# Kernel optimization log

Measured on AMD Instinct MI355X. Metric: run time of the kernel, lower is better.

## Reference

```python
import jax, jax.numpy as jnp
import numpy as np

N_NODES = 100000
DIM = 128
N_EDGES = 1600000
BN_EPS = 1e-5


def setup_inputs() -> dict:
    key = jax.random.key(0)
    ks = jax.random.split(key, 8)
    x = jax.random.normal(ks[0], (N_NODES, DIM), dtype=jnp.float32)
    ei = jax.random.randint(ks[1], (2, N_EDGES), 0, N_NODES, dtype=jnp.int32)
    # GINConv train_eps scalar
    eps = jnp.zeros((), dtype=jnp.float32)
    # MLP: Linear(dim, 2*dim) -> BN(2*dim) -> ReLU -> Dropout -> Linear(2*dim, dim) -> BN(dim) -> ReLU
    s1 = 1.0 / np.sqrt(DIM)
    s2 = 1.0 / np.sqrt(2 * DIM)
    W1 = jax.random.uniform(ks[2], (DIM, 2 * DIM), jnp.float32, -s1, s1)
    b1 = jax.random.uniform(ks[3], (2 * DIM,), jnp.float32, -s1, s1)
    W2 = jax.random.uniform(ks[4], (2 * DIM, DIM), jnp.float32, -s2, s2)
    b2 = jax.random.uniform(ks[5], (DIM,), jnp.float32, -s2, s2)
    g1 = jnp.ones((2 * DIM,), jnp.float32)
    be1 = jnp.zeros((2 * DIM,), jnp.float32)
    m1 = jax.random.normal(ks[6], (2 * DIM,), jnp.float32) * 0.1
    v1 = jnp.ones((2 * DIM,), jnp.float32)
    g2 = jnp.ones((DIM,), jnp.float32)
    be2 = jnp.zeros((DIM,), jnp.float32)
    m2 = jax.random.normal(ks[7], (DIM,), jnp.float32) * 0.1
    v2 = jnp.ones((DIM,), jnp.float32)
    return {"x": x, "eps": eps, "W1": W1, "b1": b1, "g1": g1, "be1": be1,
            "m1": m1, "v1": v1, "W2": W2, "b2": b2, "g2": g2, "be2": be2,
            "m2": m2, "v2": v2, "ei": ei}


def _bn(h, gamma, beta, mean, var):
    # BatchNorm1d in eval mode (running stats)
    return gamma * (h - mean) * jax.lax.rsqrt(var + BN_EPS) + beta


def reference(x, eps, W1, b1, g1, be1, m1, v1, W2, b2, g2, be2, m2, v2, ei):
    src, dst = ei[0], ei[1]
    # GIN aggregation: sum of neighbor (source) features scattered to destination
    agg = jax.ops.segment_sum(x[src], dst, num_segments=N_NODES)  # [N, dim]
    h = (1.0 + eps) * x + agg
    h = jax.nn.relu(_bn(h @ W1 + b1, g1, be1, m1, v1))  # [N, 2*dim]
    # Dropout is identity in eval mode
    h = jax.nn.relu(_bn(h @ W2 + b2, g2, be2, m2, v2))  # [N, dim]
    return h
```

## Files before the change

### kernel.cpp

```cpp
#include <hip/hip_runtime.h>

#define N_NODES 100000
#define DIM     128
#define HID     256
#define BN_EPS  1e-5f
#define TILES   3125
#define GEMM_GRID 256
#define BK_BITS 9
#define NBK     196
#define BKCAP   12288
#define EPB     4096

typedef _Float16     half4  __attribute__((ext_vector_type(4)));
typedef _Float16     half8  __attribute__((ext_vector_type(8)));
typedef float        f32x4  __attribute__((ext_vector_type(4)));

static __device__ __forceinline__ f32x4 mfma16h(half8 a, half8 b, f32x4 c) {
    return __builtin_amdgcn_mfma_f32_16x16x32_f16(a, b, c, 0, 0, 0);
}

__global__ __launch_bounds__(256) void cvt_kernel(const float* __restrict__ x,
                                                  _Float16* __restrict__ x16) {
    int i = blockIdx.x * 256 + threadIdx.x;
    float4 v = ((const float4*)x)[i];
    half4 o;
    o[0] = (_Float16)v.x; o[1] = (_Float16)v.y;
    o[2] = (_Float16)v.z; o[3] = (_Float16)v.w;
    ((half4*)x16)[i] = o;
}

__global__ __launch_bounds__(256) void binscatter_kernel(
    const int* __restrict__ src, const int* __restrict__ dst,
    int* __restrict__ cursor, unsigned int* __restrict__ pairs, int nE) {
    __shared__ int cnt[NBK];
    __shared__ int gbase[NBK];
    int t = threadIdx.x;
    for (int i = t; i < NBK; i += 256) cnt[i] = 0;
    __syncthreads();
    int e0 = blockIdx.x * EPB;
    int n = min(EPB, nE - e0);
    int d[16];
#pragma unroll
    for (int k = 0; k < 16; ++k) {
        int idx = t + k * 256;
        if (idx < n) {
            d[k] = dst[e0 + idx];
            atomicAdd(&cnt[d[k] >> BK_BITS], 1);
        }
    }
    __syncthreads();
    for (int i = t; i < NBK; i += 256) {
        int c = cnt[i];
        gbase[i] = c ? atomicAdd(&cursor[i], c) : 0;
    }
    __syncthreads();
    for (int i = t; i < NBK; i += 256) cnt[i] = 0;
    __syncthreads();
#pragma unroll
    for (int k = 0; k < 16; ++k) {
        int idx = t + k * 256;
        if (idx < n) {
            int b = d[k] >> BK_BITS;
            int r = atomicAdd(&cnt[b], 1);
            pairs[(long long)b * BKCAP + gbase[b] + r] =
                ((unsigned)src[e0 + idx] << BK_BITS) | ((unsigned)d[k] & 511u);
        }
    }
}

__global__ __launch_bounds__(256) void bscan_kernel(const int* __restrict__ cursor,
                                                    int* __restrict__ bbase) {
    __shared__ int tmp[256];
    int t = threadIdx.x;
    int v = (t < NBK) ? cursor[t] : 0;
    tmp[t] = v;
    __syncthreads();
    for (int s = 1; s < 256; s <<= 1) {
        int a = (t >= s) ? tmp[t - s] : 0;
        __syncthreads();
        tmp[t] += a;
        __syncthreads();
    }
    if (t < NBK) bbase[t] = tmp[t] - v;
}

__global__ __launch_bounds__(512) void bucket_fill_kernel(
    const unsigned int* __restrict__ pairs, const int* __restrict__ cursor,
    const int* __restrict__ bbase, int* __restrict__ rowptr, int* __restrict__ csr_src) {
    __shared__ int cnt[512];
    __shared__ int off[512];
    int b = blockIdx.x;
    int t = threadIdx.x;
    int nd0 = b << BK_BITS;
    int nn = min(512, N_NODES - nd0);
    int m = cursor[b];
    int base = bbase[b];
    const unsigned int* bp = pairs + (long long)b * BKCAP;
    cnt[t] = 0;
    __syncthreads();
    for (int e = t; e < m; e += 512)
        atomicAdd(&cnt[bp[e] & 511u], 1);
    __syncthreads();
    int v = cnt[t];
    off[t] = v;
    __syncthreads();
    for (int s = 1; s < 512; s <<= 1) {
        int a = (t >= s) ? off[t - s] : 0;
        __syncthreads();
        off[t] += a;
        __syncthreads();
    }
    int excl = off[t] - v;
    __syncthreads();
    off[t] = excl;
    if (t < nn) rowptr[nd0 + t] = base + excl;
    if (b == NBK - 1 && t == 0) rowptr[N_NODES] = base + m;
    cnt[t] = 0;
    __syncthreads();
    for (int e = t; e < m; e += 512) {
        unsigned int p = bp[e];
        int li = p & 511u;
        int r = atomicAdd(&cnt[li], 1);
        csr_src[base + off[li] + r] = (int)(p >> BK_BITS);
    }
}

__global__ __launch_bounds__(256) void gather_pack_kernel(
    const float* __restrict__ x, const _Float16* __restrict__ x16,
    const float* __restrict__ epsp, const int* __restrict__ rowptr,
    const int* __restrict__ csr_src, _Float16* __restrict__ h16) {
    int node = blockIdx.x * 8 + (threadIdx.x >> 5);
    int lane = threadIdx.x & 31;
    const half4* xp = (const half4*)x16;
    int beg = rowptr[node], end = rowptr[node + 1];
    float4 a0 = {0.f,0.f,0.f,0.f}, a1 = {0.f,0.f,0.f,0.f};
    float4 a2 = {0.f,0.f,0.f,0.f}, a3 = {0.f,0.f,0.f,0.f};
#define ACC4(A, V) { A.x += (float)V[0]; A.y += (float)V[1]; A.z += (float)V[2]; A.w += (float)V[3]; }
    int j = beg;
    for (; j + 4 <= end; j += 4) {
        int s0 = csr_src[j], s1 = csr_src[j+1], s2 = csr_src[j+2], s3 = csr_src[j+3];
        half4 v0 = xp[s0 * 32 + lane];
        half4 v1 = xp[s1 * 32 + lane];
        half4 v2 = xp[s2 * 32 + lane];
        half4 v3 = xp[s3 * 32 + lane];
        ACC4(a0, v0); ACC4(a1, v1); ACC4(a2, v2); ACC4(a3, v3);
    }
    for (; j < end; ++j) {
        int s = csr_src[j];
        half4 v = xp[s * 32 + lane];
        ACC4(a0, v);
    }
#undef ACC4
    float sc = 1.f + epsp[0];
    float4 xv = ((const float4*)x)[node * 32 + lane];
    half4 o;
    o[0] = (_Float16)fmaf(sc, xv.x, a0.x + a1.x + a2.x + a3.x);
    o[1] = (_Float16)fmaf(sc, xv.y, a0.y + a1.y + a2.y + a3.y);
    o[2] = (_Float16)fmaf(sc, xv.z, a0.z + a1.z + a2.z + a3.z);
    o[3] = (_Float16)fmaf(sc, xv.w, a0.w + a1.w + a2.w + a3.w);
    ((half4*)h16)[node * 32 + lane] = o;
}

__global__ __launch_bounds__(512, 2) void gemm1_kernel(
    const _Float16* __restrict__ h16, const float* __restrict__ W1,
    const float* __restrict__ b1, const float* __restrict__ g1,
    const float* __restrict__ be1, const float* __restrict__ m1,
    const float* __restrict__ v1, _Float16* __restrict__ h1p) {
    int t = threadIdx.x;
    int w = t >> 6, l = t & 63;
    int l15 = l & 15, q = l >> 4;
    int cg = w & 3, mg = w >> 2;

    half8 B1h[4][4], B1l[4][4];
    float s1v[4], sh1v[4];
#pragma unroll
    for (int nt = 0; nt < 4; ++nt) {
        int col = 64 * cg + 16 * nt + l15;
#pragma unroll
        for (int ks = 0; ks < 4; ++ks) {
            half8 bh, bl;
#pragma unroll
            for (int i = 0; i < 8; ++i) {
                float wv = W1[(32 * ks + 8 * q + i) * HID + col];
                _Float16 hh = (_Float16)wv;
                bh[i] = hh;
                bl[i] = (_Float16)(wv - (float)hh);
            }
            B1h[nt][ks] = bh; B1l[nt][ks] = bl;
        }
        float sc = g1[col] * rsqrtf(v1[col] + BN_EPS);
        s1v[nt] = sc;
        sh1v[nt] = (b1[col] - m1[col]) * sc + be1[col];
    }

    for (int tile = blockIdx.x; tile < TILES; tile += GEMM_GRID) {
        int row0 = tile * 32;
        int row = row0 + 16 * mg + l15;
        const _Float16* arow = h16 + (long long)row * DIM;
        half8 A[4];
#pragma unroll
        for (int ks = 0; ks < 4; ++ks) A[ks] = *(const half8*)(arow + 32 * ks + 8 * q);
        f32x4 acc[4];
#pragma unroll
        for (int nt = 0; nt < 4; ++nt) acc[nt] = (f32x4)(0.f);
#pragma unroll
        for (int nt = 0; nt < 4; ++nt)
#pragma unroll
            for (int ks = 0; ks < 4; ++ks) {
                acc[nt] = mfma16h(A[ks], B1h[nt][ks], acc[nt]);
                acc[nt] = mfma16h(A[ks], B1l[nt][ks], acc[nt]);
            }
#pragma unroll
        for (int nt = 0; nt < 4; ++nt) {
            int col = 64 * cg + 16 * nt + l15;
#pragma unroll
            for (int reg = 0; reg < 4; ++reg) {
                int orow = row0 + 16 * mg + 4 * q + reg;
                float vv = fmaxf(0.f, fmaf(acc[nt][reg], s1v[nt], sh1v[nt]));
                h1p[(long long)orow * HID + col] = (_Float16)vv;
            }
        }
    }
}

__global__ __launch_bounds__(512, 2) void gemm2_kernel(
    const _Float16* __restrict__ h1p, const float* __restrict__ W2,
    const float* __restrict__ b2, const float* __restrict__ g2,
    const float* __restrict__ be2, const float* __restrict__ m2,
    const float* __restrict__ v2, float* __restrict__ out) {
    int t = threadIdx.x;
    int w = t >> 6, l = t & 63;
    int l15 = l & 15, q = l >> 4;
    int cg = w & 3, mg = w >> 2;

    half8 B2h[2][8], B2l[2][8];
    float s2v[2], sh2v[2];
#pragma unroll
    for (int nt = 0; nt < 2; ++nt) {
        int col = 32 * cg + 16 * nt + l15;
#pragma unroll
        for (int ks = 0; ks < 8; ++ks) {
            half8 bh, bl;
#pragma unroll
            for (int i = 0; i < 8; ++i) {
                float wv = W2[(32 * ks + 8 * q + i) * DIM + col];
                _Float16 hh = (_Float16)wv;
                bh[i] = hh;
                bl[i] = (_Float16)(wv - (float)hh);
            }
            B2h[nt][ks] = bh; B2l[nt][ks] = bl;
        }
        float sc = g2[col] * rsqrtf(v2[col] + BN_EPS);
        s2v[nt] = sc;
        sh2v[nt] = (b2[col] - m2[col]) * sc + be2[col];
    }

    for (int tile = blockIdx.x; tile < TILES; tile += GEMM_GRID) {
        int row0 = tile * 32;
        int row = row0 + 16 * mg + l15;
        const _Float16* arow = h1p + (long long)row * HID;
        half8 A2[8];
#pragma unroll
        for (int ks = 0; ks < 8; ++ks) A2[ks] = *(const half8*)(arow + 32 * ks + 8 * q);
        f32x4 acc[2];
        acc[0] = (f32x4)(0.f); acc[1] = (f32x4)(0.f);
#pragma unroll
        for (int nt = 0; nt < 2; ++nt)
#pragma unroll
            for (int ks = 0; ks < 8; ++ks) {
                acc[nt] = mfma16h(A2[ks], B2h[nt][ks], acc[nt]);
                acc[nt] = mfma16h(A2[ks], B2l[nt][ks], acc[nt]);
            }
#pragma unroll
        for (int nt = 0; nt < 2; ++nt) {
            int col = 32 * cg + 16 * nt + l15;
#pragma unroll
            for (int reg = 0; reg < 4; ++reg) {
                int orow = row0 + 16 * mg + 4 * q + reg;
                out[(long long)orow * DIM + col] = fmaxf(0.f, fmaf(acc[nt][reg], s2v[nt], sh2v[nt]));
            }
        }
    }
}

extern "C" void kernel_launch(void* const* d_in, const int* in_sizes, int n_in,
                              void* d_out, int out_size, void* d_ws, size_t ws_size,
                              hipStream_t stream) {
    const float* x   = (const float*)d_in[0];
    const float* eps = (const float*)d_in[1];
    const float* W1  = (const float*)d_in[2];
    const float* b1  = (const float*)d_in[3];
    const float* g1  = (const float*)d_in[4];
    const float* be1 = (const float*)d_in[5];
    const float* m1  = (const float*)d_in[6];
    const float* v1  = (const float*)d_in[7];
    const float* W2  = (const float*)d_in[8];
    const float* b2  = (const float*)d_in[9];
    const float* g2  = (const float*)d_in[10];
    const float* be2 = (const float*)d_in[11];
    const float* m2  = (const float*)d_in[12];
    const float* v2  = (const float*)d_in[13];
    const int*   ei  = (const int*)d_in[14];
    int nE = in_sizes[14] / 2;
    const int* src = ei;
    const int* dst = ei + nE;

    char* ws = (char*)d_ws;
    int*          cursor  = (int*)(ws + 0);
    int*          bbase   = (int*)(ws + 1024);
    int*          rowptr  = (int*)(ws + 4096);
    int*          csr_src = (int*)(ws + 405504);
    unsigned int* pairs   = (unsigned int*)(ws + 6806528);
    _Float16*     x16     = (_Float16*)(ws + 16441344);
    _Float16*     h1p     = (_Float16*)ws;

    _Float16* h16 = (_Float16*)d_out;

    cvt_kernel<<<N_NODES * DIM / 4 / 256, 256, 0, stream>>>(x, x16);

    hipMemsetAsync(cursor, 0, NBK * sizeof(int), stream);
    binscatter_kernel<<<(nE + EPB - 1) / EPB, 256, 0, stream>>>(src, dst, cursor, pairs, nE);
    bscan_kernel<<<1, 256, 0, stream>>>(cursor, bbase);
    bucket_fill_kernel<<<NBK, 512, 0, stream>>>(pairs, cursor, bbase, rowptr, csr_src);

    gather_pack_kernel<<<N_NODES / 8, 256, 0, stream>>>(x, x16, eps, rowptr, csr_src, h16);

    gemm1_kernel<<<GEMM_GRID, 512, 0, stream>>>(h16, W1, b1, g1, be1, m1, v1, h1p);

    gemm2_kernel<<<GEMM_GRID, 512, 0, stream>>>(h1p, W2, b2, g2, be2, m2, v2, (float*)d_out);
}
```

Measured before the change: 179.1 us.

## Fuse MLP GEMMs via LDS, merge cvt into binning, drop split-fp16 weights

Both GEMMs now run in one kernel, with the hidden activation tile staged in swizzled shared memory instead of written to and reread from global memory. The fp32 to fp16 conversion runs as extra blocks of the binning kernel. The bucket-offset scan moves into bucket_fill, removing a launch. The gather uses 16 lanes with half8 loads per node. The hi/lo split-weight MFMA pair is dropped for a single fp16 weight, which halves MFMA work but lowers weight precision and may affect accuracy.

```diff
diff --git a/kernel.cpp b/kernel.cpp
--- a/kernel.cpp
+++ b/kernel.cpp
@@ -10,8 +10,9 @@
 #define NBK     196
 #define BKCAP   12288
 #define EPB     4096
-
-typedef _Float16     half4  __attribute__((ext_vector_type(4)));
+#define BIN_BLOCKS 391
+#define CVT_BLOCKS 3125
+
 typedef _Float16     half8  __attribute__((ext_vector_type(8)));
 typedef float        f32x4  __attribute__((ext_vector_type(4)));
 
@@ -19,22 +20,32 @@
     return __builtin_amdgcn_mfma_f32_16x16x32_f16(a, b, c, 0, 0, 0);
 }
 
-__global__ __launch_bounds__(256) void cvt_kernel(const float* __restrict__ x,
-                                                  _Float16* __restrict__ x16) {
-    int i = blockIdx.x * 256 + threadIdx.x;
-    float4 v = ((const float4*)x)[i];
-    half4 o;
-    o[0] = (_Float16)v.x; o[1] = (_Float16)v.y;
-    o[2] = (_Float16)v.z; o[3] = (_Float16)v.w;
-    ((half4*)x16)[i] = o;
-}
-
-__global__ __launch_bounds__(256) void binscatter_kernel(
+__global__ __launch_bounds__(256) void bin_cvt_kernel(
     const int* __restrict__ src, const int* __restrict__ dst,
-    int* __restrict__ cursor, unsigned int* __restrict__ pairs, int nE) {
+    int* __restrict__ cursor, unsigned int* __restrict__ pairs, int nE,
+    const float* __restrict__ x, _Float16* __restrict__ x16) {
+    int t = threadIdx.x;
+    if (blockIdx.x >= BIN_BLOCKS) {
+        int bc = blockIdx.x - BIN_BLOCKS;
+#pragma unroll
+        for (int k = 0; k < 4; ++k) {
+            int i = bc * 1024 + k * 256 + t;
+            float4 v = ((const float4*)x)[i];
+            half8 o8;
+            _Float16 h0 = (_Float16)v.x, h1 = (_Float16)v.y,
+                     h2 = (_Float16)v.z, h3 = (_Float16)v.w;
+            unsigned long long pk =
+                (unsigned long long)__builtin_bit_cast(unsigned short, h0)
+              | ((unsigned long long)__builtin_bit_cast(unsigned short, h1) << 16)
+              | ((unsigned long long)__builtin_bit_cast(unsigned short, h2) << 32)
+              | ((unsigned long long)__builtin_bit_cast(unsigned short, h3) << 48);
+            ((unsigned long long*)x16)[i] = pk;
+            (void)o8;
+        }
+        return;
+    }
     __shared__ int cnt[NBK];
     __shared__ int gbase[NBK];
-    int t = threadIdx.x;
     for (int i = t; i < NBK; i += 256) cnt[i] = 0;
     __syncthreads();
     int e0 = blockIdx.x * EPB;
@@ -68,33 +79,29 @@
     }
 }
 
-__global__ __launch_bounds__(256) void bscan_kernel(const int* __restrict__ cursor,
-                                                    int* __restrict__ bbase) {
-    __shared__ int tmp[256];
-    int t = threadIdx.x;
-    int v = (t < NBK) ? cursor[t] : 0;
-    tmp[t] = v;
-    __syncthreads();
-    for (int s = 1; s < 256; s <<= 1) {
-        int a = (t >= s) ? tmp[t - s] : 0;
-        __syncthreads();
-        tmp[t] += a;
-        __syncthreads();
-    }
-    if (t < NBK) bbase[t] = tmp[t] - v;
-}
-
 __global__ __launch_bounds__(512) void bucket_fill_kernel(
     const unsigned int* __restrict__ pairs, const int* __restrict__ cursor,
-    const int* __restrict__ bbase, int* __restrict__ rowptr, int* __restrict__ csr_src) {
+    int* __restrict__ rowptr, int* __restrict__ csr_src) {
     __shared__ int cnt[512];
     __shared__ int off[512];
+    __shared__ int stmp[256];
+    __shared__ int s_base;
     int b = blockIdx.x;
     int t = threadIdx.x;
+    if (t < 256) stmp[t] = (t < NBK) ? cursor[t] : 0;
+    __syncthreads();
+    for (int s = 1; s < 256; s <<= 1) {
+        int a = (t >= s && t < 256) ? stmp[t - s] : 0;
+        __syncthreads();
+        if (t < 256) stmp[t] += a;
+        __syncthreads();
+    }
+    if (t == 0) s_base = stmp[b] - cursor[b];
+    __syncthreads();
+    int base = s_base;
+    int m = cursor[b];
     int nd0 = b << BK_BITS;
     int nn = min(512, N_NODES - nd0);
-    int m = cursor[b];
-    int base = bbase[b];
     const unsigned int* bp = pairs + (long long)b * BKCAP;
     cnt[t] = 0;
     __syncthreads();
@@ -125,130 +132,92 @@
     }
 }
 
-__global__ __launch_bounds__(256) void gather_pack_kernel(
+__global__ __launch_bounds__(256) void gather_kernel(
     const float* __restrict__ x, const _Float16* __restrict__ x16,
     const float* __restrict__ epsp, const int* __restrict__ rowptr,
     const int* __restrict__ csr_src, _Float16* __restrict__ h16) {
-    int node = blockIdx.x * 8 + (threadIdx.x >> 5);
-    int lane = threadIdx.x & 31;
-    const half4* xp = (const half4*)x16;
+    int node = blockIdx.x * 16 + (threadIdx.x >> 4);
+    int lane = threadIdx.x & 15;
+    const half8* xp = (const half8*)x16;
     int beg = rowptr[node], end = rowptr[node + 1];
-    float4 a0 = {0.f,0.f,0.f,0.f}, a1 = {0.f,0.f,0.f,0.f};
-    float4 a2 = {0.f,0.f,0.f,0.f}, a3 = {0.f,0.f,0.f,0.f};
-#define ACC4(A, V) { A.x += (float)V[0]; A.y += (float)V[1]; A.z += (float)V[2]; A.w += (float)V[3]; }
+    float s0[8] = {0,0,0,0,0,0,0,0}, s1[8] = {0,0,0,0,0,0,0,0};
     int j = beg;
     for (; j + 4 <= end; j += 4) {
-        int s0 = csr_src[j], s1 = csr_src[j+1], s2 = csr_src[j+2], s3 = csr_src[j+3];
-        half4 v0 = xp[s0 * 32 + lane];
-        half4 v1 = xp[s1 * 32 + lane];
-        half4 v2 = xp[s2 * 32 + lane];
-        half4 v3 = xp[s3 * 32 + lane];
-        ACC4(a0, v0); ACC4(a1, v1); ACC4(a2, v2); ACC4(a3, v3);
+        int n0 = csr_src[j], n1 = csr_src[j+1], n2 = csr_src[j+2], n3 = csr_src[j+3];
+        half8 v0 = xp[n0 * 16 + lane];
+        half8 v1 = xp[n1 * 16 + lane];
+        half8 v2 = xp[n2 * 16 + lane];
+        half8 v3 = xp[n3 * 16 + lane];
+#pragma unroll
+        for (int i = 0; i < 8; ++i) {
+            s0[i] += (float)v0[i]; s1[i] += (float)v1[i];
+            s0[i] += (float)v2[i]; s1[i] += (float)v3[i];
+        }
     }
     for (; j < end; ++j) {
-        int s = csr_src[j];
-        half4 v = xp[s * 32 + lane];
-        ACC4(a0, v);
-    }
-#undef ACC4
+        half8 v = xp[csr_src[j] * 16 + lane];
+#pragma unroll
+        for (int i = 0; i < 8; ++i) s0[i] += (float)v[i];
+    }
     float sc = 1.f + epsp[0];
-    float4 xv = ((const float4*)x)[node * 32 + lane];
-    half4 o;
-    o[0] = (_Float16)fmaf(sc, xv.x, a0.x + a1.x + a2.x + a3.x);
-    o[1] = (_Float16)fmaf(sc, xv.y, a0.y + a1.y + a2.y + a3.y);
-    o[2] = (_Float16)fmaf(sc, xv.z, a0.z + a1.z + a2.z + a3.z);
-    o[3] = (_Float16)fmaf(sc, xv.w, a0.w + a1.w + a2.w + a3.w);
-    ((half4*)h16)[node * 32 + lane] = o;
-}
-
-__global__ __launch_bounds__(512, 2) void gemm1_kernel(
-    const _Float16* __restrict__ h16, const float* __restrict__ W1,
-    const float* __restrict__ b1, const float* __restrict__ g1,
-    const float* __restrict__ be1, const float* __restrict__ m1,
-    const float* __restrict__ v1, _Float16* __restrict__ h1p) {
+    float4 xa = ((const float4*)x)[node * 32 + lane * 2];
+    float4 xb = ((const float4*)x)[node * 32 + lane * 2 + 1];
+    half8 o;
+    o[0] = (_Float16)fmaf(sc, xa.x, s0[0] + s1[0]);
+    o[1] = (_Float16)fmaf(sc, xa.y, s0[1] + s1[1]);
+    o[2] = (_Float16)fmaf(sc, xa.z, s0[2] + s1[2]);
+    o[3] = (_Float16)fmaf(sc, xa.w, s0[3] + s1[3]);
+    o[4] = (_Float16)fmaf(sc, xb.x, s0[4] + s1[4]);
+    o[5] = (_Float16)fmaf(sc, xb.y, s0[5] + s1[5]);
+    o[6] = (_Float16)fmaf(sc, xb.z, s0[6] + s1[6]);
+    o[7] = (_Float16)fmaf(sc, xb.w, s0[7] + s1[7]);
+    ((half8*)h16)[node * 16 + lane] = o;
+}
+
+__global__ __launch_bounds__(512, 2) void mlp_fused_kernel(
+    const _Float16* __restrict__ h16,
+    const float* __restrict__ W1, const float* __restrict__ b1,
+    const float* __restrict__ g1, const float* __restrict__ be1,
+    const float* __restrict__ m1, const float* __restrict__ v1,
+    const float* __restrict__ W2, const float* __restrict__ b2,
+    const float* __restrict__ g2, const float* __restrict__ be2,
+    const float* __restrict__ m2, const float* __restrict__ v2,
+    float* __restrict__ out) {
+    __shared__ _Float16 sh1[32 * HID];
     int t = threadIdx.x;
     int w = t >> 6, l = t & 63;
     int l15 = l & 15, q = l >> 4;
     int cg = w & 3, mg = w >> 2;
 
-    half8 B1h[4][4], B1l[4][4];
+    half8 B1[4][4];
     float s1v[4], sh1v[4];
 #pragma unroll
     for (int nt = 0; nt < 4; ++nt) {
         int col = 64 * cg + 16 * nt + l15;
 #pragma unroll
         for (int ks = 0; ks < 4; ++ks) {
-            half8 bh, bl;
-#pragma unroll
-            for (int i = 0; i < 8; ++i) {
-                float wv = W1[(32 * ks + 8 * q + i) * HID + col];
-                _Float16 hh = (_Float16)wv;
-                bh[i] = hh;
-                bl[i] = (_Float16)(wv - (float)hh);
-            }
-            B1h[nt][ks] = bh; B1l[nt][ks] = bl;
+            half8 bh;
+#pragma unroll
+            for (int i = 0; i < 8; ++i)
+                bh[i] = (_Float16)W1[(32 * ks + 8 * q + i) * HID + col];
+            B1[nt][ks] = bh;
         }
         float sc = g1[col] * rsqrtf(v1[col] + BN_EPS);
         s1v[nt] = sc;
         sh1v[nt] = (b1[col] - m1[col]) * sc + be1[col];
     }
-
-    for (int tile = blockIdx.x; tile < TILES; tile += GEMM_GRID) {
-        int row0 = tile * 32;
-        int row = row0 + 16 * mg + l15;
-        const _Float16* arow = h16 + (long long)row * DIM;
-        half8 A[4];
-#pragma unroll
-        for (int ks = 0; ks < 4; ++ks) A[ks] = *(const half8*)(arow + 32 * ks + 8 * q);
-        f32x4 acc[4];
-#pragma unroll
-        for (int nt = 0; nt < 4; ++nt) acc[nt] = (f32x4)(0.f);
-#pragma unroll
-        for (int nt = 0; nt < 4; ++nt)
-#pragma unroll
-            for (int ks = 0; ks < 4; ++ks) {
-                acc[nt] = mfma16h(A[ks], B1h[nt][ks], acc[nt]);
-                acc[nt] = mfma16h(A[ks], B1l[nt][ks], acc[nt]);
-            }
-#pragma unroll
-        for (int nt = 0; nt < 4; ++nt) {
-            int col = 64 * cg + 16 * nt + l15;
-#pragma unroll
-            for (int reg = 0; reg < 4; ++reg) {
-                int orow = row0 + 16 * mg + 4 * q + reg;
-                float vv = fmaxf(0.f, fmaf(acc[nt][reg], s1v[nt], sh1v[nt]));
-                h1p[(long long)orow * HID + col] = (_Float16)vv;
-            }
-        }
-    }
-}
-
-__global__ __launch_bounds__(512, 2) void gemm2_kernel(
-    const _Float16* __restrict__ h1p, const float* __restrict__ W2,
-    const float* __restrict__ b2, const float* __restrict__ g2,
-    const float* __restrict__ be2, const float* __restrict__ m2,
-    const float* __restrict__ v2, float* __restrict__ out) {
-    int t = threadIdx.x;
-    int w = t >> 6, l = t & 63;
-    int l15 = l & 15, q = l >> 4;
-    int cg = w & 3, mg = w >> 2;
-
-    half8 B2h[2][8], B2l[2][8];
+    half8 B2[2][8];
     float s2v[2], sh2v[2];
 #pragma unroll
     for (int nt = 0; nt < 2; ++nt) {
         int col = 32 * cg + 16 * nt + l15;
 #pragma unroll
         for (int ks = 0; ks < 8; ++ks) {
-            half8 bh, bl;
-#pragma unroll
-            for (int i = 0; i < 8; ++i) {
-                float wv = W2[(32 * ks + 8 * q + i) * DIM + col];
-                _Float16 hh = (_Float16)wv;
-                bh[i] = hh;
-                bl[i] = (_Float16)(wv - (float)hh);
-            }
-            B2h[nt][ks] = bh; B2l[nt][ks] = bl;
+            half8 bh;
+#pragma unroll
+            for (int i = 0; i < 8; ++i)
+                bh[i] = (_Float16)W2[(32 * ks + 8 * q + i) * DIM + col];
+            B2[nt][ks] = bh;
         }
         float sc = g2[col] * rsqrtf(v2[col] + BN_EPS);
         s2v[nt] = sc;
@@ -257,27 +226,53 @@
 
     for (int tile = blockIdx.x; tile < TILES; tile += GEMM_GRID) {
         int row0 = tile * 32;
-        int row = row0 + 16 * mg + l15;
-        const _Float16* arow = h1p + (long long)row * HID;
+        const _Float16* arow = h16 + (long long)(row0 + 16 * mg + l15) * DIM;
+        half8 A[4];
+#pragma unroll
+        for (int ks = 0; ks < 4; ++ks) A[ks] = *(const half8*)(arow + 32 * ks + 8 * q);
+        f32x4 acc[4];
+#pragma unroll
+        for (int nt = 0; nt < 4; ++nt) acc[nt] = (f32x4)(0.f);
+#pragma unroll
+        for (int nt = 0; nt < 4; ++nt)
+#pragma unroll
+            for (int ks = 0; ks < 4; ++ks)
+                acc[nt] = mfma16h(A[ks], B1[nt][ks], acc[nt]);
+#pragma unroll
+        for (int nt = 0; nt < 4; ++nt) {
+            int col = 64 * cg + 16 * nt + l15;
+#pragma unroll
+            for (int reg = 0; reg < 4; ++reg) {
+                int row = 16 * mg + 4 * q + reg;
+                float vv = fmaxf(0.f, fmaf(acc[nt][reg], s1v[nt], sh1v[nt]));
+                sh1[row * HID + (col ^ ((row & 7) << 3))] = (_Float16)vv;
+            }
+        }
+        __syncthreads();
         half8 A2[8];
-#pragma unroll
-        for (int ks = 0; ks < 8; ++ks) A2[ks] = *(const half8*)(arow + 32 * ks + 8 * q);
-        f32x4 acc[2];
-        acc[0] = (f32x4)(0.f); acc[1] = (f32x4)(0.f);
+        {
+            int row = 16 * mg + l15;
+            int sx = (row & 7) << 3;
+#pragma unroll
+            for (int ks = 0; ks < 8; ++ks)
+                A2[ks] = *(const half8*)&sh1[row * HID + ((32 * ks + 8 * q) ^ sx)];
+        }
+        __syncthreads();
+        f32x4 acc2[2];
+        acc2[0] = (f32x4)(0.f); acc2[1] = (f32x4)(0.f);
 #pragma unroll
         for (int nt = 0; nt < 2; ++nt)
 #pragma unroll
-            for (int ks = 0; ks < 8; ++ks) {
-                acc[nt] = mfma16h(A2[ks], B2h[nt][ks], acc[nt]);
-                acc[nt] = mfma16h(A2[ks], B2l[nt][ks], acc[nt]);
-            }
+            for (int ks = 0; ks < 8; ++ks)
+                acc2[nt] = mfma16h(A2[ks], B2[nt][ks], acc2[nt]);
 #pragma unroll
         for (int nt = 0; nt < 2; ++nt) {
             int col = 32 * cg + 16 * nt + l15;
 #pragma unroll
             for (int reg = 0; reg < 4; ++reg) {
                 int orow = row0 + 16 * mg + 4 * q + reg;
-                out[(long long)orow * DIM + col] = fmaxf(0.f, fmaf(acc[nt][reg], s2v[nt], sh2v[nt]));
+                out[(long long)orow * DIM + col] =
+                    fmaxf(0.f, fmaf(acc2[nt][reg], s2v[nt], sh2v[nt]));
             }
         }
     }
@@ -307,25 +302,19 @@
 
     char* ws = (char*)d_ws;
     int*          cursor  = (int*)(ws + 0);
-    int*          bbase   = (int*)(ws + 1024);
     int*          rowptr  = (int*)(ws + 4096);
     int*          csr_src = (int*)(ws + 405504);
     unsigned int* pairs   = (unsigned int*)(ws + 6806528);
     _Float16*     x16     = (_Float16*)(ws + 16441344);
-    _Float16*     h1p     = (_Float16*)ws;
-
-    _Float16* h16 = (_Float16*)d_out;
-
-    cvt_kernel<<<N_NODES * DIM / 4 / 256, 256, 0, stream>>>(x, x16);
+    _Float16*     h16     = (_Float16*)(ws + 42041344);
 
     hipMemsetAsync(cursor, 0, NBK * sizeof(int), stream);
-    binscatter_kernel<<<(nE + EPB - 1) / EPB, 256, 0, stream>>>(src, dst, cursor, pairs, nE);
-    bscan_kernel<<<1, 256, 0, stream>>>(cursor, bbase);
-    bucket_fill_kernel<<<NBK, 512, 0, stream>>>(pairs, cursor, bbase, rowptr, csr_src);
-
-    gather_pack_kernel<<<N_NODES / 8, 256, 0, stream>>>(x, x16, eps, rowptr, csr_src, h16);
-
-    gemm1_kernel<<<GEMM_GRID, 512, 0, stream>>>(h16, W1, b1, g1, be1, m1, v1, h1p);
-
-    gemm2_kernel<<<GEMM_GRID, 512, 0, stream>>>(h1p, W2, b2, g2, be2, m2, v2, (float*)d_out);
-}
+    bin_cvt_kernel<<<BIN_BLOCKS + CVT_BLOCKS, 256, 0, stream>>>(src, dst, cursor, pairs, nE,
+                                                                x, x16);
+    bucket_fill_kernel<<<NBK, 512, 0, stream>>>(pairs, cursor, rowptr, csr_src);
+
+    gather_kernel<<<N_NODES / 16, 256, 0, stream>>>(x, x16, eps, rowptr, csr_src, h16);
+
+    mlp_fused_kernel<<<GEMM_GRID, 512, 0, stream>>>(h16, W1, b1, g1, be1, m1, v1,
+                                                    W2, b2, g2, be2, m2, v2, (float*)d_out);
+}
```

Measured after the change: 153.7 us. 14.2% less time.
